# Optimization experiments

Hardware: AMD Instinct MI355X
Metric: run time of the kernel (lower is better)

## Reference

```python
import jax, jax.numpy as jnp
import numpy as np

BN_EPS = 1e-5
N_NODES = 100000
N_EDGES = 1600000
F_IN = 128
F_HID = 256
N_ITEMS = 128


def setup_inputs() -> dict:
    key = jax.random.key(0)
    ks = jax.random.split(key, 6)
    return {
        "node_feature": jax.random.normal(ks[0], (N_NODES, F_IN), jnp.float32),
        "edge_index": jax.random.randint(ks[1], (2, N_EDGES), 0, N_NODES, jnp.int64),
        "items_ready_to_cache": jnp.arange(N_ITEMS, dtype=jnp.int64),
        "gcn_w": jax.random.normal(ks[2], (F_IN, F_HID), jnp.float32) / np.sqrt(F_IN),
        "gcn_b": jnp.zeros((F_HID,), jnp.float32),
        "bn_gamma": jnp.ones((F_HID,), jnp.float32),
        "bn_beta": jnp.zeros((F_HID,), jnp.float32),
        "emb_table": jax.random.normal(ks[3], (F_IN, F_IN), jnp.float32),
        "proj_w": jax.random.normal(ks[4], (F_HID, F_IN), jnp.float32) / np.sqrt(F_HID),
        "proj_b": jnp.zeros((F_IN,), jnp.float32),
    }


def _gcn_conv(x, edge_index, w, b, n_nodes):
    # PyG GCNConv: add self-loops, symmetric normalization, scatter-add to target.
    loop = jnp.arange(n_nodes, dtype=edge_index.dtype)
    src = jnp.concatenate([edge_index[0], loop])
    dst = jnp.concatenate([edge_index[1], loop])
    h = x @ w                                  # [N, F_HID]
    deg = jax.ops.segment_sum(jnp.ones_like(dst, dtype=h.dtype), dst,
                              num_segments=n_nodes)
    dinv = jnp.where(deg > 0, jax.lax.rsqrt(deg), 0.0)
    norm = dinv[src] * dinv[dst]               # [E+N]
    msgs = h[src] * norm[:, None]              # gather + scale  [E+N, F_HID]
    out = jax.ops.segment_sum(msgs, dst, num_segments=n_nodes)  # scatter-add
    return out + b


def reference(node_feature, edge_index, items_ready_to_cache, gcn_w, gcn_b,
              bn_gamma, bn_beta, emb_table, proj_w, proj_b):
    n_nodes = node_feature.shape[0]
    x = _gcn_conv(node_feature, edge_index, gcn_w, gcn_b, n_nodes)
    # BatchNorm1d in training mode: batch stats (biased variance)
    mean = jnp.mean(x, axis=0)
    var = jnp.mean((x - mean) ** 2, axis=0)
    x = bn_gamma * (x - mean) * jax.lax.rsqrt(var + BN_EPS) + bn_beta
    x = jax.nn.relu(x)
    rsu_embedding = x[0:1] @ proj_w + proj_b   # [1, F_IN]
    # item_id_to_index collapses indices to arange(len(items))
    n_items = items_ready_to_cache.shape[0]
    items_embeddings = emb_table[jnp.arange(n_items)]  # [n_items, F_IN]
    scores = items_embeddings @ rsu_embedding[0]       # [n_items]
    return scores, rsu_embedding
```

## Files before the change

kernel.cpp:

```cpp
#include <hip/hip_runtime.h>
#include <hip/hip_bf16.h>


#define THREADS 256
#define CHUNK 32

__global__ __launch_bounds__(THREADS) void deg_rank_kernel(const int* __restrict__ ei,
                                                           int* __restrict__ deg,
                                                           int* __restrict__ rank,
                                                           int E, int N) {
    int e4 = (blockIdx.x * THREADS + threadIdx.x) * 4;
    if (e4 + 3 < E) {
        int4 d = *(const int4*)(ei + E + e4);
        int4 r;
        r.x = ((unsigned)d.x < (unsigned)N) ? atomicAdd(&deg[d.x], 1) : 0;
        r.y = ((unsigned)d.y < (unsigned)N) ? atomicAdd(&deg[d.y], 1) : 0;
        r.z = ((unsigned)d.z < (unsigned)N) ? atomicAdd(&deg[d.z], 1) : 0;
        r.w = ((unsigned)d.w < (unsigned)N) ? atomicAdd(&deg[d.w], 1) : 0;
        *(int4*)(rank + e4) = r;
    } else if (e4 < E) {
        for (int u = e4; u < E; ++u) {
            unsigned d = (unsigned)ei[E + u];
            rank[u] = (d < (unsigned)N) ? atomicAdd(&deg[d], 1) : 0;
        }
    }
}

__global__ __launch_bounds__(THREADS) void scan1_kernel(const int* __restrict__ deg,
                                                        int* __restrict__ rowptr,
                                                        int* __restrict__ bsum,
                                                        float* __restrict__ dinv, int n) {
    __shared__ int sh[THREADS];
    const int t = threadIdx.x, b = blockIdx.x;
    const int base = b * 1024 + t * 4;
    int v0 = (base + 0 < n) ? deg[base + 0] : 0;
    int v1 = (base + 1 < n) ? deg[base + 1] : 0;
    int v2 = (base + 2 < n) ? deg[base + 2] : 0;
    int v3 = (base + 3 < n) ? deg[base + 3] : 0;
    if (base + 0 < n) dinv[base + 0] = rsqrtf((float)(v0 + 1));
    if (base + 1 < n) dinv[base + 1] = rsqrtf((float)(v1 + 1));
    if (base + 2 < n) dinv[base + 2] = rsqrtf((float)(v2 + 1));
    if (base + 3 < n) dinv[base + 3] = rsqrtf((float)(v3 + 1));
    const int local = v0 + v1 + v2 + v3;
    sh[t] = local;
    __syncthreads();
    int run = local;
    for (int off = 1; off < THREADS; off <<= 1) {
        int add = (t >= off) ? sh[t - off] : 0;
        __syncthreads();
        run += add;
        sh[t] = run;
        __syncthreads();
    }
    const int excl = run - local;
    if (base + 0 < n) rowptr[base + 0] = excl;
    if (base + 1 < n) rowptr[base + 1] = excl + v0;
    if (base + 2 < n) rowptr[base + 2] = excl + v0 + v1;
    if (base + 3 < n) rowptr[base + 3] = excl + v0 + v1 + v2;
    if (t == 0) bsum[b] = sh[THREADS - 1];
}

__global__ __launch_bounds__(THREADS) void scan2_kernel(const int* __restrict__ bsum,
                                                        int* __restrict__ boff, int nb,
                                                        float* __restrict__ colsumS,
                                                        float* __restrict__ G,
                                                        int* __restrict__ workctr) {
    __shared__ int sh[THREADS];
    const int t = threadIdx.x;
    const int local = (t < nb) ? bsum[t] : 0;
    sh[t] = local;
    __syncthreads();
    int run = local;
    for (int off = 1; off < THREADS; off <<= 1) {
        int add = (t >= off) ? sh[t - off] : 0;
        __syncthreads();
        run += add;
        sh[t] = run;
        __syncthreads();
    }
    boff[t] = run - local;
    if (t < 128) colsumS[t] = 0.f;
    if (t == 0) *workctr = 0;
    for (int u = t; u < 16384; u += THREADS) G[u] = 0.f;
}

__global__ __launch_bounds__(THREADS) void scatter_kernel(const int* __restrict__ ei,
                                                          const int* __restrict__ rowptr,
                                                          const int* __restrict__ boff,
                                                          const int* __restrict__ rank,
                                                          int* __restrict__ csr,
                                                          int E, int N) {
    int e4 = (blockIdx.x * THREADS + threadIdx.x) * 4;
    if (e4 + 3 < E) {
        int4 d = *(const int4*)(ei + E + e4);
        int4 s = *(const int4*)(ei + e4);
        int4 r = *(const int4*)(rank + e4);
        if ((unsigned)d.x < (unsigned)N) {
            int p = rowptr[d.x] + boff[d.x >> 10] + r.x;
            if ((unsigned)p < (unsigned)E) csr[p] = s.x;
        }
        if ((unsigned)d.y < (unsigned)N) {
            int p = rowptr[d.y] + boff[d.y >> 10] + r.y;
            if ((unsigned)p < (unsigned)E) csr[p] = s.y;
        }
        if ((unsigned)d.z < (unsigned)N) {
            int p = rowptr[d.z] + boff[d.z >> 10] + r.z;
            if ((unsigned)p < (unsigned)E) csr[p] = s.z;
        }
        if ((unsigned)d.w < (unsigned)N) {
            int p = rowptr[d.w] + boff[d.w >> 10] + r.w;
            if ((unsigned)p < (unsigned)E) csr[p] = s.w;
        }
    } else if (e4 < E) {
        for (int u = e4; u < E; ++u) {
            unsigned d = (unsigned)ei[E + u];
            if (d < (unsigned)N) {
                int p = rowptr[d] + boff[d >> 10] + rank[u];
                if ((unsigned)p < (unsigned)E) csr[p] = ei[u];
            }
        }
    }
}

__global__ __launch_bounds__(512) void agg_syrk_kernel(
        const float* __restrict__ x, const int* __restrict__ rowptr,
        const int* __restrict__ boff, const int* __restrict__ csr,
        const float* __restrict__ dinv, int* __restrict__ workctr,
        float* __restrict__ Gpart, float* __restrict__ colsumS,
        float* __restrict__ agg0, int n, int E, int NC) {
    __shared__ float Asm[CHUNK * 132];
    __shared__ int sh_c;
    const int t = threadIdx.x;
    const int lane = t & 63, wv = t >> 6;
    const int p0 = (t >> 5) * 8;
    const int q0 = (t & 31) * 4;
    const float* xl = x + lane * 2;

    float acc[8][4];
#pragma unroll
    for (int i = 0; i < 8; ++i)
#pragma unroll
        for (int j = 0; j < 4; ++j) acc[i][j] = 0.f;
    float s_acc = 0.f;

    for (;;) {
        if (t == 0) sh_c = atomicAdd(workctr, 1);
        __syncthreads();
        const int c = sh_c;
        if (c >= NC) break;

        for (int rr = 0; rr < CHUNK / 8; ++rr) {
            const int r = wv * (CHUNK / 8) + rr;
            const int i = c * CHUNK + r;
            float ax = 0.f, ay = 0.f;
            if (i < n) {
                const int e0 = rowptr[i] + boff[i >> 10];
                const int e1 = (i + 1 < n) ? rowptr[i + 1] + boff[(i + 1) >> 10] : E;
                const float di = dinv[i];
                const float2 xs = *(const float2*)(xl + (size_t)i * 128);
                ax = di * xs.x; ay = di * xs.y;
                int e = e0;
                for (; e + 8 <= e1; e += 8) {
                    int ss[8]; float ww[8]; float2 pv[8];
#pragma unroll
                    for (int u = 0; u < 8; ++u) {
                        int s = csr[e + u];
                        ss[u] = ((unsigned)s < (unsigned)n) ? s : 0;
                    }
#pragma unroll
                    for (int u = 0; u < 8; ++u) ww[u] = dinv[ss[u]];
#pragma unroll
                    for (int u = 0; u < 8; ++u)
                        pv[u] = *(const float2*)(xl + (size_t)ss[u] * 128);
#pragma unroll
                    for (int u = 0; u < 8; ++u) {
                        ax = fmaf(ww[u], pv[u].x, ax);
                        ay = fmaf(ww[u], pv[u].y, ay);
                    }
                }
                for (; e < e1; ++e) {
                    int s = csr[e];
                    s = ((unsigned)s < (unsigned)n) ? s : 0;
                    float w = dinv[s];
                    float2 p = *(const float2*)(xl + (size_t)s * 128);
                    ax = fmaf(w, p.x, ax);
                    ay = fmaf(w, p.y, ay);
                }
                ax *= di; ay *= di;
            }
            *(float2*)(Asm + r * 132 + lane * 2) = make_float2(ax, ay);
        }
        __syncthreads();

        if (c == 0 && t < 32)
            *(float4*)(agg0 + t * 4) = *(const float4*)(Asm + t * 4);

#pragma unroll 4
        for (int r = 0; r < CHUNK; ++r) {
            const float* row = Asm + r * 132;
            float4 a0 = *(const float4*)(row + p0);
            float4 a1 = *(const float4*)(row + p0 + 4);
            float4 bq = *(const float4*)(row + q0);
            float ap[8] = {a0.x, a0.y, a0.z, a0.w, a1.x, a1.y, a1.z, a1.w};
            float aq[4] = {bq.x, bq.y, bq.z, bq.w};
#pragma unroll
            for (int pp = 0; pp < 8; ++pp)
#pragma unroll
                for (int qq = 0; qq < 4; ++qq)
                    acc[pp][qq] = fmaf(ap[pp], aq[qq], acc[pp][qq]);
        }
        if (t < 128) {
            float sa = 0.f;
#pragma unroll 4
            for (int r = 0; r < CHUNK; ++r) sa += Asm[r * 132 + t];
            s_acc += sa;
        }
        __syncthreads();
    }

    float* gp = Gpart + (size_t)blockIdx.x * 16384;
#pragma unroll
    for (int pp = 0; pp < 8; ++pp)
        *(float4*)(gp + (p0 + pp) * 128 + q0) =
            make_float4(acc[pp][0], acc[pp][1], acc[pp][2], acc[pp][3]);
    if (t < 128) atomicAdd(&colsumS[t], s_acc);
}

__global__ __launch_bounds__(THREADS) void greduce_kernel(const float* __restrict__ Gpart,
                                                          float* __restrict__ G, int NB) {
    const int seg = blockIdx.x >> 4;
    const int i4 = (blockIdx.x & 15) * THREADS + threadIdx.x;
    const int b0 = (seg * NB) / 8, b1 = ((seg + 1) * NB) / 8;
    float4 a = make_float4(0.f, 0.f, 0.f, 0.f);
    for (int b = b0; b < b1; ++b) {
        float4 v = *(const float4*)(Gpart + (size_t)b * 16384 + i4 * 4);
        a.x += v.x; a.y += v.y; a.z += v.z; a.w += v.w;
    }
    atomicAdd(&G[i4 * 4 + 0], a.x);
    atomicAdd(&G[i4 * 4 + 1], a.y);
    atomicAdd(&G[i4 * 4 + 2], a.z);
    atomicAdd(&G[i4 * 4 + 3], a.w);
}

__global__ __launch_bounds__(THREADS) void stats_kernel(
        const float* __restrict__ G, const float* __restrict__ W,
        const float* __restrict__ bias, const float* __restrict__ colsumS,
        const float* __restrict__ agg0, float* __restrict__ colsum,
        float* __restrict__ colsumsq, float* __restrict__ row0, int n) {
    __shared__ float wsm[128];
    __shared__ float red[THREADS], red2[THREADS], red3[THREADS];
    const int t = threadIdx.x, j = blockIdx.x;
    if (t < 128) wsm[t] = W[t * 256 + j];
    __syncthreads();
    float part = 0.f;
    const float wq = wsm[t & 127];
    const int pbase = t >> 7;
#pragma unroll 8
    for (int u = 0; u < 64; ++u)
        part = fmaf(G[u * 256 + t], wsm[pbase + u * 2], part);
    red[t] = part * wq;
    red2[t] = (t < 128) ? colsumS[t] * wsm[t] : 0.f;
    red3[t] = (t < 128) ? agg0[t] * wsm[t] : 0.f;
    __syncthreads();
    for (int s = 128; s > 0; s >>= 1) {
        if (t < s) { red[t] += red[t + s]; red2[t] += red2[t + s]; red3[t] += red3[t + s]; }
        __syncthreads();
    }
    if (t == 0) {
        const float b = bias[j];
        const float sw = red2[0];
        colsum[j]   = sw + (float)n * b;
        colsumsq[j] = red[0] + 2.f * b * sw + (float)n * b * b;
        row0[j]     = red3[0] + b;
    }
}

__global__ __launch_bounds__(THREADS) void finalize_kernel(
        const float* __restrict__ colsum, const float* __restrict__ colsumsq,
        const float* __restrict__ row0, const float* __restrict__ gamma,
        const float* __restrict__ beta, const float* __restrict__ proj_w,
        const float* __restrict__ proj_b, const float* __restrict__ emb,
        float* __restrict__ out, int n_nodes, int n_items) {
    __shared__ float x0[256];
    __shared__ float rsu[128];
    const int t = threadIdx.x;
    const float invn = 1.0f / (float)n_nodes;
    {
        float mean = colsum[t] * invn;
        float var = colsumsq[t] * invn - mean * mean;
        float r = rsqrtf(var + 1e-5f);
        float v = gamma[t] * (row0[t] - mean) * r + beta[t];
        x0[t] = v > 0.f ? v : 0.f;
    }
    __syncthreads();
    if (t < 128) {
        float sacc = proj_b[t];
        for (int c = 0; c < 256; ++c) sacc = fmaf(x0[c], proj_w[c * 128 + t], sacc);
        rsu[t] = sacc;
        out[128 + t] = sacc;
    }
    __syncthreads();
    if (t < n_items) {
        float sacc = 0.f;
        for (int j = 0; j < 128; ++j) sacc = fmaf(emb[t * 128 + j], rsu[j], sacc);
        out[t] = sacc;
    }
}

extern "C" void kernel_launch(void* const* d_in, const int* in_sizes, int n_in,
                              void* d_out, int out_size, void* d_ws, size_t ws_size,
                              hipStream_t stream) {
    const float* node_feature = (const float*)d_in[0];
    const int*   edge_index   = (const int*)d_in[1];
    const float* gcn_w  = (const float*)d_in[3];
    const float* gcn_b  = (const float*)d_in[4];
    const float* bn_g   = (const float*)d_in[5];
    const float* bn_b   = (const float*)d_in[6];
    const float* emb    = (const float*)d_in[7];
    const float* proj_w = (const float*)d_in[8];
    const float* proj_b = (const float*)d_in[9];
    float* out = (float*)d_out;

    const int N = in_sizes[0] / 128;
    const int E = in_sizes[1] / 2;
    const int n_items = in_sizes[2];

    char* base = (char*)d_ws;
    size_t off = 0;
    auto alloc = [&](size_t bytes) -> void* {
        void* p = (void*)(base + off);
        off += (bytes + 255) & ~(size_t)255;
        return p;
    };
    int*   deg      = (int*)alloc((size_t)N * 4);
    int*   rank     = (int*)alloc((size_t)E * 4);
    int*   rowptr   = (int*)alloc((size_t)N * 4);
    int*   bsum     = (int*)alloc(256 * 4);
    int*   boff     = (int*)alloc(256 * 4);
    float* dinv     = (float*)alloc((size_t)N * 4);
    int*   csr      = (int*)alloc((size_t)E * 4);
    float* colsumS  = (float*)alloc(128 * 4);
    float* agg0     = (float*)alloc(128 * 4);
    float* G        = (float*)alloc(16384 * 4);
    float* colsum   = (float*)alloc(256 * 4);
    float* colsumsq = (float*)alloc(256 * 4);
    float* row0     = (float*)alloc(256 * 4);
    int*   workctr  = (int*)alloc(256);
    int NB = (int)((ws_size > off) ? ((ws_size - off) / (16384 * 4)) : 0);
    if (NB > 1024) NB = 1024;
    if (NB < 8) NB = 8;
    float* Gpart    = (float*)alloc((size_t)NB * 16384 * 4);

    const int nbE4 = (E / 4 + THREADS - 1) / THREADS;
    const int nchunks = (N + 1023) >> 10;
    const int NC = (N + CHUNK - 1) / CHUNK;

    hipMemsetAsync(deg, 0, (size_t)N * 4, stream);

    deg_rank_kernel<<<nbE4, THREADS, 0, stream>>>(edge_index, deg, rank, E, N);
    scan1_kernel<<<nchunks, THREADS, 0, stream>>>(deg, rowptr, bsum, dinv, N);
    scan2_kernel<<<1, THREADS, 0, stream>>>(bsum, boff, nchunks, colsumS, G, workctr);
    scatter_kernel<<<nbE4, THREADS, 0, stream>>>(edge_index, rowptr, boff, rank, csr, E, N);
    agg_syrk_kernel<<<NB, 512, 0, stream>>>(node_feature, rowptr, boff, csr, dinv,
                                            workctr, Gpart, colsumS, agg0, N, E, NC);
    greduce_kernel<<<128, THREADS, 0, stream>>>(Gpart, G, NB);
    stats_kernel<<<256, THREADS, 0, stream>>>(G, gcn_w, gcn_b, colsumS, agg0,
                                              colsum, colsumsq, row0, N);
    finalize_kernel<<<1, THREADS, 0, stream>>>(colsum, colsumsq, row0, bn_g, bn_b,
                                               proj_w, proj_b, emb, out, N, n_items);
}
```

Before: 443.6 us.

## Split aggregation from SYRK, merge scan and finalize kernels via last-block counters

The fused aggregation+Gram kernel is split in two. The aggregation kernel now writes the full normalized aggregate matrix to workspace, and a separate SYRK kernel re-reads it in 32-row chunks and atomically accumulates directly into G, which removes the per-block Gpart buffers and the greduce pass. The two scan kernels and the stats/finalize kernels are each merged using a last-block atomic counter, and the zeroing of G, colsumS and the counters is folded into the initial memset. This trades fewer launches and no partial-G reduction for an extra 51 MB write plus read of the aggregate, and for many more float atomics on G.

```diff
diff --git a/kernel.cpp b/kernel.cpp
--- a/kernel.cpp
+++ b/kernel.cpp
@@ -3,7 +3,6 @@
 
 
 #define THREADS 256
-#define CHUNK 32
 
 __global__ __launch_bounds__(THREADS) void deg_rank_kernel(const int* __restrict__ ei,
                                                            int* __restrict__ deg,
@@ -26,11 +25,14 @@
     }
 }
 
-__global__ __launch_bounds__(THREADS) void scan1_kernel(const int* __restrict__ deg,
-                                                        int* __restrict__ rowptr,
-                                                        int* __restrict__ bsum,
-                                                        float* __restrict__ dinv, int n) {
+__global__ __launch_bounds__(THREADS) void scan_kernel(const int* __restrict__ deg,
+                                                       int* __restrict__ rowptr,
+                                                       int* __restrict__ bsum,
+                                                       int* __restrict__ boff,
+                                                       float* __restrict__ dinv,
+                                                       int* __restrict__ ctr, int n) {
     __shared__ int sh[THREADS];
+    __shared__ int isLast;
     const int t = threadIdx.x, b = blockIdx.x;
     const int base = b * 1024 + t * 4;
     int v0 = (base + 0 < n) ? deg[base + 0] : 0;
@@ -57,31 +59,28 @@
     if (base + 1 < n) rowptr[base + 1] = excl + v0;
     if (base + 2 < n) rowptr[base + 2] = excl + v0 + v1;
     if (base + 3 < n) rowptr[base + 3] = excl + v0 + v1 + v2;
-    if (t == 0) bsum[b] = sh[THREADS - 1];
-}
-
-__global__ __launch_bounds__(THREADS) void scan2_kernel(const int* __restrict__ bsum,
-                                                        int* __restrict__ boff, int nb,
-                                                        float* __restrict__ colsumS,
-                                                        float* __restrict__ G,
-                                                        int* __restrict__ workctr) {
-    __shared__ int sh[THREADS];
-    const int t = threadIdx.x;
-    const int local = (t < nb) ? bsum[t] : 0;
-    sh[t] = local;
-    __syncthreads();
-    int run = local;
-    for (int off = 1; off < THREADS; off <<= 1) {
-        int add = (t >= off) ? sh[t - off] : 0;
-        __syncthreads();
-        run += add;
-        sh[t] = run;
-        __syncthreads();
-    }
-    boff[t] = run - local;
-    if (t < 128) colsumS[t] = 0.f;
-    if (t == 0) *workctr = 0;
-    for (int u = t; u < 16384; u += THREADS) G[u] = 0.f;
+    if (t == 0) {
+        bsum[b] = sh[THREADS - 1];
+        __threadfence();
+        isLast = (atomicAdd(ctr, 1) == (int)gridDim.x - 1);
+    }
+    __syncthreads();
+    if (isLast) {
+        __threadfence();
+        const int nb = gridDim.x;
+        const int lv = (t < nb) ? bsum[t] : 0;
+        sh[t] = lv;
+        __syncthreads();
+        int r2 = lv;
+        for (int off = 1; off < THREADS; off <<= 1) {
+            int add = (t >= off) ? sh[t - off] : 0;
+            __syncthreads();
+            r2 += add;
+            sh[t] = r2;
+            __syncthreads();
+        }
+        boff[t] = r2 - lv;
+    }
 }
 
 __global__ __launch_bounds__(THREADS) void scatter_kernel(const int* __restrict__ ei,
@@ -122,20 +121,62 @@
     }
 }
 
-__global__ __launch_bounds__(512) void agg_syrk_kernel(
-        const float* __restrict__ x, const int* __restrict__ rowptr,
-        const int* __restrict__ boff, const int* __restrict__ csr,
-        const float* __restrict__ dinv, int* __restrict__ workctr,
-        float* __restrict__ Gpart, float* __restrict__ colsumS,
-        float* __restrict__ agg0, int n, int E, int NC) {
-    __shared__ float Asm[CHUNK * 132];
-    __shared__ int sh_c;
+__global__ __launch_bounds__(THREADS) void agg_kernel(const float* __restrict__ x,
+                                                      const int* __restrict__ rowptr,
+                                                      const int* __restrict__ boff,
+                                                      const int* __restrict__ csr,
+                                                      const float* __restrict__ dinv,
+                                                      float* __restrict__ agg,
+                                                      int n, int E) {
+    const int lane = threadIdx.x & 63;
+    const int wid  = blockIdx.x * (THREADS >> 6) + (threadIdx.x >> 6);
+    const int nw   = gridDim.x * (THREADS >> 6);
+    const float* xl = x + lane * 2;
+    for (int i = wid; i < n; i += nw) {
+        const int e0 = rowptr[i] + boff[i >> 10];
+        const int e1 = (i + 1 < n) ? rowptr[i + 1] + boff[(i + 1) >> 10] : E;
+        const float di = dinv[i];
+        const float2 xs = *(const float2*)(xl + (size_t)i * 128);
+        float ax = di * xs.x, ay = di * xs.y;
+        int e = e0;
+        for (; e + 8 <= e1; e += 8) {
+            int ss[8]; float ww[8]; float2 pv[8];
+#pragma unroll
+            for (int u = 0; u < 8; ++u) {
+                int s = csr[e + u];
+                ss[u] = ((unsigned)s < (unsigned)n) ? s : 0;
+            }
+#pragma unroll
+            for (int u = 0; u < 8; ++u) ww[u] = dinv[ss[u]];
+#pragma unroll
+            for (int u = 0; u < 8; ++u)
+                pv[u] = *(const float2*)(xl + (size_t)ss[u] * 128);
+#pragma unroll
+            for (int u = 0; u < 8; ++u) {
+                ax = fmaf(ww[u], pv[u].x, ax);
+                ay = fmaf(ww[u], pv[u].y, ay);
+            }
+        }
+        for (; e < e1; ++e) {
+            int s = csr[e];
+            s = ((unsigned)s < (unsigned)n) ? s : 0;
+            float w = dinv[s];
+            float2 p = *(const float2*)(xl + (size_t)s * 128);
+            ax = fmaf(w, p.x, ax);
+            ay = fmaf(w, p.y, ay);
+        }
+        *(float2*)(agg + (size_t)i * 128 + lane * 2) = make_float2(di * ax, di * ay);
+    }
+}
+
+__global__ __launch_bounds__(512) void syrk_kernel(const float* __restrict__ agg,
+                                                   float* __restrict__ G,
+                                                   float* __restrict__ colsumS,
+                                                   int n, int NCHK) {
+    __shared__ float Asm[32 * 132];
     const int t = threadIdx.x;
-    const int lane = t & 63, wv = t >> 6;
     const int p0 = (t >> 5) * 8;
     const int q0 = (t & 31) * 4;
-    const float* xl = x + lane * 2;
-
     float acc[8][4];
 #pragma unroll
     for (int i = 0; i < 8; ++i)
@@ -143,60 +184,19 @@
         for (int j = 0; j < 4; ++j) acc[i][j] = 0.f;
     float s_acc = 0.f;
 
-    for (;;) {
-        if (t == 0) sh_c = atomicAdd(workctr, 1);
-        __syncthreads();
-        const int c = sh_c;
-        if (c >= NC) break;
-
-        for (int rr = 0; rr < CHUNK / 8; ++rr) {
-            const int r = wv * (CHUNK / 8) + rr;
-            const int i = c * CHUNK + r;
-            float ax = 0.f, ay = 0.f;
-            if (i < n) {
-                const int e0 = rowptr[i] + boff[i >> 10];
-                const int e1 = (i + 1 < n) ? rowptr[i + 1] + boff[(i + 1) >> 10] : E;
-                const float di = dinv[i];
-                const float2 xs = *(const float2*)(xl + (size_t)i * 128);
-                ax = di * xs.x; ay = di * xs.y;
-                int e = e0;
-                for (; e + 8 <= e1; e += 8) {
-                    int ss[8]; float ww[8]; float2 pv[8];
-#pragma unroll
-                    for (int u = 0; u < 8; ++u) {
-                        int s = csr[e + u];
-                        ss[u] = ((unsigned)s < (unsigned)n) ? s : 0;
-                    }
-#pragma unroll
-                    for (int u = 0; u < 8; ++u) ww[u] = dinv[ss[u]];
-#pragma unroll
-                    for (int u = 0; u < 8; ++u)
-                        pv[u] = *(const float2*)(xl + (size_t)ss[u] * 128);
-#pragma unroll
-                    for (int u = 0; u < 8; ++u) {
-                        ax = fmaf(ww[u], pv[u].x, ax);
-                        ay = fmaf(ww[u], pv[u].y, ay);
-                    }
-                }
-                for (; e < e1; ++e) {
-                    int s = csr[e];
-                    s = ((unsigned)s < (unsigned)n) ? s : 0;
-                    float w = dinv[s];
-                    float2 p = *(const float2*)(xl + (size_t)s * 128);
-                    ax = fmaf(w, p.x, ax);
-                    ay = fmaf(w, p.y, ay);
-                }
-                ax *= di; ay *= di;
-            }
-            *(float2*)(Asm + r * 132 + lane * 2) = make_float2(ax, ay);
-        }
-        __syncthreads();
-
-        if (c == 0 && t < 32)
-            *(float4*)(agg0 + t * 4) = *(const float4*)(Asm + t * 4);
-
+    for (int c = blockIdx.x; c < NCHK; c += gridDim.x) {
+#pragma unroll
+        for (int u = 0; u < 2; ++u) {
+            int f4 = t * 2 + u;
+            int r = f4 >> 5, c4 = f4 & 31;
+            int gr = c * 32 + r;
+            float4 v = make_float4(0.f, 0.f, 0.f, 0.f);
+            if (gr < n) v = *(const float4*)(agg + (size_t)gr * 128 + c4 * 4);
+            *(float4*)(Asm + r * 132 + c4 * 4) = v;
+        }
+        __syncthreads();
 #pragma unroll 4
-        for (int r = 0; r < CHUNK; ++r) {
+        for (int r = 0; r < 32; ++r) {
             const float* row = Asm + r * 132;
             float4 a0 = *(const float4*)(row + p0);
             float4 a1 = *(const float4*)(row + p0 + 4);
@@ -212,43 +212,33 @@
         if (t < 128) {
             float sa = 0.f;
 #pragma unroll 4
-            for (int r = 0; r < CHUNK; ++r) sa += Asm[r * 132 + t];
+            for (int r = 0; r < 32; ++r) sa += Asm[r * 132 + t];
             s_acc += sa;
         }
         __syncthreads();
     }
-
-    float* gp = Gpart + (size_t)blockIdx.x * 16384;
-#pragma unroll
-    for (int pp = 0; pp < 8; ++pp)
-        *(float4*)(gp + (p0 + pp) * 128 + q0) =
-            make_float4(acc[pp][0], acc[pp][1], acc[pp][2], acc[pp][3]);
+#pragma unroll
+    for (int pp = 0; pp < 8; ++pp) {
+        atomicAdd(&G[(p0 + pp) * 128 + q0 + 0], acc[pp][0]);
+        atomicAdd(&G[(p0 + pp) * 128 + q0 + 1], acc[pp][1]);
+        atomicAdd(&G[(p0 + pp) * 128 + q0 + 2], acc[pp][2]);
+        atomicAdd(&G[(p0 + pp) * 128 + q0 + 3], acc[pp][3]);
+    }
     if (t < 128) atomicAdd(&colsumS[t], s_acc);
 }
 
-__global__ __launch_bounds__(THREADS) void greduce_kernel(const float* __restrict__ Gpart,
-                                                          float* __restrict__ G, int NB) {
-    const int seg = blockIdx.x >> 4;
-    const int i4 = (blockIdx.x & 15) * THREADS + threadIdx.x;
-    const int b0 = (seg * NB) / 8, b1 = ((seg + 1) * NB) / 8;
-    float4 a = make_float4(0.f, 0.f, 0.f, 0.f);
-    for (int b = b0; b < b1; ++b) {
-        float4 v = *(const float4*)(Gpart + (size_t)b * 16384 + i4 * 4);
-        a.x += v.x; a.y += v.y; a.z += v.z; a.w += v.w;
-    }
-    atomicAdd(&G[i4 * 4 + 0], a.x);
-    atomicAdd(&G[i4 * 4 + 1], a.y);
-    atomicAdd(&G[i4 * 4 + 2], a.z);
-    atomicAdd(&G[i4 * 4 + 3], a.w);
-}
-
-__global__ __launch_bounds__(THREADS) void stats_kernel(
+__global__ __launch_bounds__(THREADS) void stats_fin_kernel(
         const float* __restrict__ G, const float* __restrict__ W,
         const float* __restrict__ bias, const float* __restrict__ colsumS,
-        const float* __restrict__ agg0, float* __restrict__ colsum,
-        float* __restrict__ colsumsq, float* __restrict__ row0, int n) {
+        const float* __restrict__ agg, float* __restrict__ colsum,
+        float* __restrict__ colsumsq, float* __restrict__ row0,
+        const float* __restrict__ gamma, const float* __restrict__ beta,
+        const float* __restrict__ proj_w, const float* __restrict__ proj_b,
+        const float* __restrict__ emb, float* __restrict__ out,
+        int* __restrict__ ctr, int n, int n_items) {
     __shared__ float wsm[128];
     __shared__ float red[THREADS], red2[THREADS], red3[THREADS];
+    __shared__ int isLast;
     const int t = threadIdx.x, j = blockIdx.x;
     if (t < 128) wsm[t] = W[t * 256 + j];
     __syncthreads();
@@ -260,7 +250,7 @@
         part = fmaf(G[u * 256 + t], wsm[pbase + u * 2], part);
     red[t] = part * wq;
     red2[t] = (t < 128) ? colsumS[t] * wsm[t] : 0.f;
-    red3[t] = (t < 128) ? agg0[t] * wsm[t] : 0.f;
+    red3[t] = (t < 128) ? agg[t] * wsm[t] : 0.f;
     __syncthreads();
     for (int s = 128; s > 0; s >>= 1) {
         if (t < s) { red[t] += red[t + s]; red2[t] += red2[t + s]; red3[t] += red3[t + s]; }
@@ -272,19 +262,15 @@
         colsum[j]   = sw + (float)n * b;
         colsumsq[j] = red[0] + 2.f * b * sw + (float)n * b * b;
         row0[j]     = red3[0] + b;
-    }
-}
-
-__global__ __launch_bounds__(THREADS) void finalize_kernel(
-        const float* __restrict__ colsum, const float* __restrict__ colsumsq,
-        const float* __restrict__ row0, const float* __restrict__ gamma,
-        const float* __restrict__ beta, const float* __restrict__ proj_w,
-        const float* __restrict__ proj_b, const float* __restrict__ emb,
-        float* __restrict__ out, int n_nodes, int n_items) {
+        __threadfence();
+        isLast = (atomicAdd(ctr, 1) == (int)gridDim.x - 1);
+    }
+    __syncthreads();
+    if (!isLast) return;
+    __threadfence();
     __shared__ float x0[256];
     __shared__ float rsu[128];
-    const int t = threadIdx.x;
-    const float invn = 1.0f / (float)n_nodes;
+    const float invn = 1.0f / (float)n;
     {
         float mean = colsum[t] * invn;
         float var = colsumsq[t] * invn - mean * mean;
@@ -302,7 +288,7 @@
     __syncthreads();
     if (t < n_items) {
         float sacc = 0.f;
-        for (int j = 0; j < 128; ++j) sacc = fmaf(emb[t * 128 + j], rsu[j], sacc);
+        for (int jj = 0; jj < 128; ++jj) sacc = fmaf(emb[t * 128 + jj], rsu[jj], sacc);
         out[t] = sacc;
     }
 }
@@ -333,39 +319,38 @@
         return p;
     };
     int*   deg      = (int*)alloc((size_t)N * 4);
+    float* G        = (float*)alloc(16384 * 4);
+    float* colsumS  = (float*)alloc(128 * 4);
+    int*   ctrs     = (int*)alloc(256);
+    const size_t zero_bytes = off;
     int*   rank     = (int*)alloc((size_t)E * 4);
     int*   rowptr   = (int*)alloc((size_t)N * 4);
     int*   bsum     = (int*)alloc(256 * 4);
     int*   boff     = (int*)alloc(256 * 4);
     float* dinv     = (float*)alloc((size_t)N * 4);
     int*   csr      = (int*)alloc((size_t)E * 4);
-    float* colsumS  = (float*)alloc(128 * 4);
-    float* agg0     = (float*)alloc(128 * 4);
-    float* G        = (float*)alloc(16384 * 4);
     float* colsum   = (float*)alloc(256 * 4);
     float* colsumsq = (float*)alloc(256 * 4);
     float* row0     = (float*)alloc(256 * 4);
-    int*   workctr  = (int*)alloc(256);
-    int NB = (int)((ws_size > off) ? ((ws_size - off) / (16384 * 4)) : 0);
-    if (NB > 1024) NB = 1024;
-    if (NB < 8) NB = 8;
-    float* Gpart    = (float*)alloc((size_t)NB * 16384 * 4);
+    float* agg      = (float*)alloc((size_t)N * 128 * 4);
+    (void)ws_size;
 
     const int nbE4 = (E / 4 + THREADS - 1) / THREADS;
     const int nchunks = (N + 1023) >> 10;
-    const int NC = (N + CHUNK - 1) / CHUNK;
-
-    hipMemsetAsync(deg, 0, (size_t)N * 4, stream);
+    const int NCHK = (N + 31) / 32;
+
+    hipMemsetAsync(deg, 0, zero_bytes, stream);
 
     deg_rank_kernel<<<nbE4, THREADS, 0, stream>>>(edge_index, deg, rank, E, N);
-    scan1_kernel<<<nchunks, THREADS, 0, stream>>>(deg, rowptr, bsum, dinv, N);
-    scan2_kernel<<<1, THREADS, 0, stream>>>(bsum, boff, nchunks, colsumS, G, workctr);
-    scatter_kernel<<<nbE4, THREADS, 0, stream>>>(edge_index, rowptr, boff, rank, csr, E, N);
-    agg_syrk_kernel<<<NB, 512, 0, stream>>>(node_feature, rowptr, boff, csr, dinv,
-                                            workctr, Gpart, colsumS, agg0, N, E, NC);
-    greduce_kernel<<<128, THREADS, 0, stream>>>(Gpart, G, NB);
-    stats_kernel<<<256, THREADS, 0, stream>>>(G, gcn_w, gcn_b, colsumS, agg0,
-                                              colsum, colsumsq, row0, N);
-    finalize_kernel<<<1, THREADS, 0, stream>>>(colsum, colsumsq, row0, bn_g, bn_b,
-                                               proj_w, proj_b, emb, out, N, n_items);
-}
+    scan_kernel<<<nchunks, THREADS, 0, stream>>>(deg, rowptr, bsum, boff, dinv,
+                                                 &ctrs[0], N);
+    scatter_kernel<<<nbE4, THREADS, 0, stream>>>(edge_index, rowptr, boff, rank,
+                                                 csr, E, N);
+    agg_kernel<<<2048, THREADS, 0, stream>>>(node_feature, rowptr, boff, csr, dinv,
+                                             agg, N, E);
+    syrk_kernel<<<512, 512, 0, stream>>>(agg, G, colsumS, N, NCHK);
+    stats_fin_kernel<<<256, THREADS, 0, stream>>>(G, gcn_w, gcn_b, colsumS, agg,
+                                                  colsum, colsumsq, row0, bn_g, bn_b,
+                                                  proj_w, proj_b, emb, out,
+                                                  &ctrs[1], N, n_items);
+}
```

After: 524.0 us. 18.1% more time.
